# Kernel tuning notes

Measured on AMD Instinct MI355X. Metric: run time of the kernel, lower is better.

Reference implementation:

```python
import jax, jax.numpy as jnp
import numpy as np
from jax import lax

EDGES = [(11,12),(11,23),(12,24),(23,24),(23,25),(25,27),(24,26),(26,28),(11,13),(13,15),(12,14),(14,16)]
J = 33

def _build_neighbors():
    nb = [[j] for j in range(J)]
    for a, b in EDGES:
        nb[a].append(b); nb[b].append(a)
    K = max(len(n) for n in nb)
    idx = np.zeros((J, K), np.int32)
    msk = np.zeros((J, K), np.float32)
    for j, n in enumerate(nb):
        idx[j, :len(n)] = n; msk[j, :len(n)] = 1.0
    return jnp.asarray(idx), jnp.asarray(msk)

NBR_IDX, NBR_MASK = _build_neighbors()
BN_EPS = 1e-5

def conv(x, w, b):
    y = lax.conv_general_dilated(x, w, (1, 1), 'SAME', dimension_numbers=('NCHW', 'OIHW', 'NCHW'))
    return y + b[None, :, None, None]

def bn(x, g, b):
    # eval-mode BatchNorm with running_mean=0, running_var=1
    s = g / jnp.sqrt(1.0 + BN_EPS)
    return x * s[None, :, None, None] + b[None, :, None, None]

def maxpool2(x):
    return lax.reduce_window(x, -jnp.inf, lax.max, (1, 1, 2, 2), (1, 1, 2, 2), 'VALID')

def deconv2x2(x, w, b):
    # ConvTranspose2d(k=2, s=2): w is [Cin, Cout, 2, 2]
    y = jnp.einsum('bcij,codk->boidjk', x, w)
    B, O, H, _, W, _ = y.shape
    return y.reshape(B, O, 2 * H, 2 * W) + b[None, :, None, None]

def forward(x, conv1_w, conv1_b, bn1_g, bn1_b, conv2_w, conv2_b, bn2_g, bn2_b,
            conv3_w, conv3_b, bn3_g, bn3_b, conv4_w, conv4_b, bn4_g, bn4_b,
            dc1_w, dc1_b, dc2_w, dc2_b, head_w, head_b, proj_w, proj_b,
            msg_w, msg_b, gru_w_ih, gru_w_hh, gru_b_ih, gru_b_hh,
            refine_w, refine_b, vis_w1, vis_b1, vis_w2, vis_b2):
    relu = jax.nn.relu
    h = bn(relu(conv(x, conv1_w, conv1_b)), bn1_g, bn1_b)
    h = bn(relu(conv(h, conv2_w, conv2_b)), bn2_g, bn2_b)
    h = maxpool2(h)
    h = bn(relu(conv(h, conv3_w, conv3_b)), bn3_g, bn3_b)
    h = maxpool2(h)
    enc = bn(relu(conv(h, conv4_w, conv4_b)), bn4_g, bn4_b)  # [B,256,H/4,W/4]
    f = relu(deconv2x2(enc, dc1_w, dc1_b))
    feat_map = relu(deconv2x2(f, dc2_w, dc2_b))  # [B,64,H,W]
    init_hm = jax.nn.sigmoid(conv(feat_map, head_w, head_b))  # [B,J,H,W]
    B, Jn, H, W = init_hm.shape
    sm = jax.nn.softmax(init_hm.reshape(B, Jn, H * W) / 0.1, axis=-1).reshape(B, Jn, H, W)
    w_idx = jnp.linspace(0.0, 1.0, W)
    h_idx = jnp.linspace(0.0, 1.0, H)
    pred_x = (sm.sum(-2) * w_idx).sum(-1)  # [B,J] in [0,1]
    pred_y = (sm.sum(-1) * h_idx).sum(-1)
    # grid_sample bilinear, align_corners=True: grid=(2p-1) -> pixel coord p*(dim-1)
    ix = pred_x * (W - 1)
    iy = pred_y * (H - 1)
    x0 = jnp.clip(jnp.floor(ix), 0, W - 1)
    y0 = jnp.clip(jnp.floor(iy), 0, H - 1)
    wx = ix - x0
    wy = iy - y0
    x0i = x0.astype(jnp.int32); x1i = jnp.clip(x0i + 1, 0, W - 1)
    y0i = y0.astype(jnp.int32); y1i = jnp.clip(y0i + 1, 0, H - 1)
    fm = feat_map.transpose(0, 2, 3, 1)  # [B,H,W,C]
    bidx = jnp.arange(B)[:, None]
    v00 = fm[bidx, y0i, x0i]; v01 = fm[bidx, y0i, x1i]
    v10 = fm[bidx, y1i, x0i]; v11 = fm[bidx, y1i, x1i]
    wx = wx[..., None]; wy = wy[..., None]
    joint = (v00 * (1 - wx) * (1 - wy) + v01 * wx * (1 - wy)
             + v10 * (1 - wx) * wy + v11 * wx * wy)  # [B,J,64]
    joint_feats = joint @ proj_w.T + proj_b
    # SkeletonGNN (all joints read original joint_feats -> fully parallel)
    gathered = joint_feats[:, NBR_IDX, :]  # [B,J,K,D]
    lin = gathered @ msg_w.T + msg_b
    m = NBR_MASK[None, :, :, None]
    msgs = (lin * m).sum(2) / NBR_MASK.sum(1)[None, :, None]  # [B,J,D]
    gi = msgs @ gru_w_ih.T + gru_b_ih
    gh = joint_feats @ gru_w_hh.T + gru_b_hh
    D = joint_feats.shape[-1]
    ir, iz, inn = gi[..., :D], gi[..., D:2 * D], gi[..., 2 * D:]
    hr, hz, hn = gh[..., :D], gh[..., D:2 * D], gh[..., 2 * D:]
    r = jax.nn.sigmoid(ir + hr)
    z = jax.nn.sigmoid(iz + hz)
    n = jnp.tanh(inn + r * hn)
    refined_feats = (1 - z) * n + z * joint_feats
    refined_bias = refined_feats.mean(-1)[:, :, None, None]
    refined_hm = jax.nn.sigmoid(conv(init_hm, refine_w, refine_b) + refined_bias)
    # visibility head: adaptive avg pool to 4x4 (enc HW divisible by 4), eval dropout = identity
    eB, eC, eH, eW = enc.shape
    p = enc.reshape(eB, eC, 4, eH // 4, 4, eW // 4).mean((3, 5))  # [B,256,4,4]
    v = jax.nn.relu(p.reshape(eB, -1) @ vis_w1.T + vis_b1)
    vis_pred = jax.nn.sigmoid(v @ vis_w2.T + vis_b2)
    return refined_hm, vis_pred

def setup_inputs() -> dict:
    key = jax.random.key(0)
    ks = iter(jax.random.split(key, 64))
    def w(shape, s=0.05):
        return (jax.random.normal(next(ks), shape, dtype=jnp.float32) * s)
    inp = {
        'x': jax.random.normal(next(ks), (16, 3, 256, 256), dtype=jnp.float32),
        'conv1_w': w((32, 3, 3, 3)), 'conv1_b': w((32,)), 'bn1_g': jnp.ones((32,)), 'bn1_b': jnp.zeros((32,)),
        'conv2_w': w((64, 32, 3, 3)), 'conv2_b': w((64,)), 'bn2_g': jnp.ones((64,)), 'bn2_b': jnp.zeros((64,)),
        'conv3_w': w((128, 64, 3, 3)), 'conv3_b': w((128,)), 'bn3_g': jnp.ones((128,)), 'bn3_b': jnp.zeros((128,)),
        'conv4_w': w((256, 128, 3, 3)), 'conv4_b': w((256,)), 'bn4_g': jnp.ones((256,)), 'bn4_b': jnp.zeros((256,)),
        'dc1_w': w((256, 128, 2, 2)), 'dc1_b': w((128,)),
        'dc2_w': w((128, 64, 2, 2)), 'dc2_b': w((64,)),
        'head_w': w((33, 64, 1, 1)), 'head_b': w((33,)),
        'proj_w': w((64, 64)), 'proj_b': w((64,)),
        'msg_w': w((64, 64)), 'msg_b': w((64,)),
        'gru_w_ih': w((192, 64)), 'gru_w_hh': w((192, 64)),
        'gru_b_ih': w((192,)), 'gru_b_hh': w((192,)),
        'refine_w': w((33, 33, 3, 3)), 'refine_b': w((33,)),
        'vis_w1': w((256, 256 * 16)), 'vis_b1': w((256,)),
        'vis_w2': w((33, 256)), 'vis_b2': w((33,)),
    }
    return inp

def reference(x, conv1_w, conv1_b, bn1_g, bn1_b, conv2_w, conv2_b, bn2_g, bn2_b,
              conv3_w, conv3_b, bn3_g, bn3_b, conv4_w, conv4_b, bn4_g, bn4_b,
              dc1_w, dc1_b, dc2_w, dc2_b, head_w, head_b, proj_w, proj_b,
              msg_w, msg_b, gru_w_ih, gru_w_hh, gru_b_ih, gru_b_hh,
              refine_w, refine_b, vis_w1, vis_b1, vis_w2, vis_b2):
    return forward(x, conv1_w, conv1_b, bn1_g, bn1_b, conv2_w, conv2_b, bn2_g, bn2_b,
                   conv3_w, conv3_b, bn3_g, bn3_b, conv4_w, conv4_b, bn4_g, bn4_b,
                   dc1_w, dc1_b, dc2_w, dc2_b, head_w, head_b, proj_w, proj_b,
                   msg_w, msg_b, gru_w_ih, gru_w_hh, gru_b_ih, gru_b_hh,
                   refine_w, refine_b, vis_w1, vis_b1, vis_w2, vis_b2)
```

## Files before the change

kernel.cpp:

```cpp
#include <hip/hip_runtime.h>
#include <hip/hip_bf16.h>
#include <math.h>

#define BN_RS 0.99999500003749977f

typedef __attribute__((ext_vector_type(8))) __bf16 bf16x8;
typedef __attribute__((ext_vector_type(4))) float f32x4;

union U16 { uint4 u; bf16x8 v; __hip_bfloat16 h[8]; };

__device__ __forceinline__ float sigf(float v) { return 1.0f / (1.0f + expf(-v)); }

__global__ __launch_bounds__(256)
void repack_conv_w_k(const float* __restrict__ w, __hip_bfloat16* __restrict__ wb,
                     int taps, int Co, int Ci, int CoT, int Kp)
{
    int i = blockIdx.x * 256 + threadIdx.x;
    int tot = taps * CoT * Kp;
    if (i >= tot) return;
    int k = i % Kp, n = (i / Kp) % CoT, t = i / (Kp * CoT);
    float v = (n < Co && k < Ci) ? w[((long)n * Ci + k) * taps + t] : 0.0f;
    wb[i] = __float2bfloat16(v);
}
__global__ __launch_bounds__(256)
void repack_deconv_w_k(const float* __restrict__ w, __hip_bfloat16* __restrict__ wb,
                       int Co, int Ci)
{
    int i = blockIdx.x * 256 + threadIdx.x;
    int tot = 4 * Co * Ci;
    if (i >= tot) return;
    int k = i % Ci, n = (i / Ci) % Co, q = i / (Ci * Co);
    wb[i] = __float2bfloat16(w[((long)k * Co + n) * 4 + q]);
}

__global__ __launch_bounds__(256)
void zero_halo_k(__hip_bfloat16* __restrict__ buf, int H, int W, int C, int B)
{
    const int P = W + 2;
    const long per = (long)(2 * P + 2 * H) * C;
    long idx = (long)blockIdx.x * 256 + threadIdx.x;
    if (idx >= per * B) return;
    int b = (int)(idx / per);
    long r = idx % per;
    long off;
    if (r < (long)2 * P * C) {
        int row = (r >= (long)P * C) ? (H + 1) : 0;
        long r2 = r % ((long)P * C);
        off = (((long)b * (H + 2) + row) * P) * C + r2;
    } else {
        long r2 = r - (long)2 * P * C;
        int row = 1 + (int)(r2 / (2 * C));
        int side = (int)((r2 / C) & 1);
        int ch = (int)(r2 % C);
        off = (((long)b * (H + 2) + row) * P + (side ? (W + 1) : 0)) * C + ch;
    }
    buf[off] = __float2bfloat16(0.0f);
}

__global__ __launch_bounds__(256)
void conv1_k(const float* __restrict__ x, const float* __restrict__ w,
             const float* __restrict__ cb, const float* __restrict__ g,
             const float* __restrict__ bb, __hip_bfloat16* __restrict__ out)
{
    __shared__ float sw[216];
    const int tid = threadIdx.x;
    const int b = blockIdx.z >> 2, cg = blockIdx.z & 3, co0 = cg * 8;
    for (int i = tid; i < 216; i += 256) {
        int t = i % 9, co = (i / 9) % 8, ci = i / 72;
        sw[i] = w[((co0 + co) * 3 + ci) * 9 + t];
    }
    __syncthreads();
    const int tx = tid & 15, ty = tid >> 4;
    const int y = blockIdx.y * 16 + ty;
    const int xs = blockIdx.x * 64 + tx;
    float acc[4][8];
#pragma unroll
    for (int p = 0; p < 4; ++p)
#pragma unroll
        for (int c = 0; c < 8; ++c) acc[p][c] = 0.0f;
    for (int ci = 0; ci < 3; ++ci) {
        const float* plane = x + ((long)b * 3 + ci) * 65536;
#pragma unroll
        for (int t = 0; t < 9; ++t) {
            const int dy = t / 3 - 1, dx = t % 3 - 1;
            const int yy = y + dy;
            if ((unsigned)yy < 256u) {
                const float* row = plane + yy * 256;
                float wsr[8];
#pragma unroll
                for (int c = 0; c < 8; ++c) wsr[c] = sw[ci * 72 + c * 9 + t];
#pragma unroll
                for (int p = 0; p < 4; ++p) {
                    const int xx = xs + p * 16 + dx;
                    const float v = ((unsigned)xx < 256u) ? row[xx] : 0.0f;
#pragma unroll
                    for (int c = 0; c < 8; ++c) acc[p][c] = fmaf(v, wsr[c], acc[p][c]);
                }
            }
        }
    }
#pragma unroll
    for (int p = 0; p < 4; ++p) {
        U16 o;
#pragma unroll
        for (int c = 0; c < 8; ++c) {
            const int cc = co0 + c;
            float v = fmaxf(acc[p][c] + cb[cc], 0.0f) * (g[cc] * BN_RS) + bb[cc];
            o.h[c] = __float2bfloat16(v);
        }
        *(uint4*)(void*)(out + ((long)b * 2130048L + ((long)y * 258 + xs + p * 16) * 32) + co0) = o.u;
    }
}

template<int MODE, int NI>
__global__ __launch_bounds__(256)
void mfma_conv_k(const __hip_bfloat16* __restrict__ in,
                 const __hip_bfloat16* __restrict__ wb,
                 const float* __restrict__ cbias,
                 const float* __restrict__ bng, const float* __restrict__ bnb,
                 const float* __restrict__ ebias,
                 __hip_bfloat16* __restrict__ out_bf, float* __restrict__ out_f32,
                 int H, int W, int Cin, int PIT, long bstride, long obstride, int OPIT,
                 int CoutT, int CG, int S)
{
    extern __shared__ float ltr[];
    const int tid = threadIdx.x;
    const int wid = tid >> 6, lane = tid & 63;
    const int ln = lane & 15, kg = lane >> 4;
    const int u = blockIdx.x * 4 + wid;
    const int y = u / S, x0 = (u % S) * 64;
    const int b = blockIdx.z / CG, cg = blockIdx.z % CG;
    const int co0 = cg * 64;
    const int KC = Cin >> 5;

    f32x4 acc[4][NI];
#pragma unroll
    for (int i = 0; i < 4; ++i)
#pragma unroll
        for (int j = 0; j < NI; ++j) acc[i][j] = f32x4{0.f, 0.f, 0.f, 0.f};

    constexpr int NT = (MODE == 1) ? 1 : 9;
    for (int kc = 0; kc < KC; ++kc) {
        const int kofs = kc * 32 + kg * 8;
#pragma unroll
        for (int t = 0; t < NT; ++t) {
            const int dy = (MODE == 1) ? 0 : (t / 3 - 1);
            const int dx = (MODE == 1) ? 0 : (t % 3 - 1);
            bf16x8 wfr[NI];
#pragma unroll
            for (int ni = 0; ni < NI; ++ni)
                wfr[ni] = *(const bf16x8*)(const void*)(wb + ((long)t * CoutT + co0 + ni * 16 + ln) * Cin + kofs);
            U16 av[4];
            const long rowb = (long)b * bstride + (long)(y + dy) * PIT * Cin + kofs;
#pragma unroll
            for (int mi = 0; mi < 4; ++mi)
                av[mi].u = *(const uint4*)(const void*)(in + rowb + (long)(x0 + mi * 16 + ln + dx) * Cin);
#pragma unroll
            for (int mi = 0; mi < 4; ++mi)
#pragma unroll
                for (int ni = 0; ni < NI; ++ni)
                    acc[mi][ni] = __builtin_amdgcn_mfma_f32_16x16x32_bf16(av[mi].v, wfr[ni], acc[mi][ni], 0, 0, 0);
        }
    }

    if constexpr (MODE == 0) {
#pragma unroll
        for (int mi = 0; mi < 4; ++mi) {
#pragma unroll
            for (int r = 0; r < 4; ++r) {
                const int px = x0 + mi * 16 + kg * 4 + r;
                const long pb = (long)b * obstride + ((long)y * OPIT + px) * CoutT + co0;
#pragma unroll
                for (int ni = 0; ni < NI; ++ni) {
                    const int c = co0 + ni * 16 + ln;
                    float v = acc[mi][ni][r] + cbias[c];
                    v = fmaxf(v, 0.0f) * (bng[c] * BN_RS) + bnb[c];
                    out_bf[pb + ni * 16 + ln] = __float2bfloat16(v);
                }
            }
        }
    } else {
        float* wt = ltr + wid * (48 * 67);
#pragma unroll
        for (int mi = 0; mi < 4; ++mi) {
#pragma unroll
            for (int r = 0; r < 4; ++r) {
                const int pxl = mi * 16 + kg * 4 + r;
#pragma unroll
                for (int ni = 0; ni < NI; ++ni) {
                    const int c = ni * 16 + ln;
                    float v = acc[mi][ni][r];
                    if constexpr (MODE == 1) {
                        v = sigf(v + ((c < 33) ? cbias[c] : 0.0f));
                        out_bf[(long)b * obstride + ((long)y * OPIT + x0 + pxl) * CoutT + c] =
                            (c < 33) ? __float2bfloat16(v) : __float2bfloat16(0.0f);
                    } else {
                        float eb = (c < 33) ? (cbias[c] + ebias[b * 33 + c]) : 0.0f;
                        v = sigf(v + eb);
                    }
                    wt[c * 67 + pxl] = v;
                }
            }
        }
        const long o32 = ((long)b * 33) * H * W + (long)y * W + x0 + lane;
        for (int c = 0; c < 33; ++c)
            out_f32[o32 + (long)c * H * W] = wt[c * 67 + lane];
    }
}

__global__ __launch_bounds__(256)
void mfma_deconv_k(const __hip_bfloat16* __restrict__ in,
                   const __hip_bfloat16* __restrict__ wb,
                   const float* __restrict__ bias,
                   __hip_bfloat16* __restrict__ out,
                   int H, int W, int Cin, int CoutT, int CG, int S)
{
    const int tid = threadIdx.x;
    const int wid = tid >> 6, lane = tid & 63;
    const int ln = lane & 15, kg = lane >> 4;
    const int u = blockIdx.x * 4 + wid;
    const int y = u / S, x0 = (u % S) * 64;
    const int b = blockIdx.z / CG, cg = blockIdx.z % CG;
    const int co0 = cg * 64;
    const int KC = Cin >> 5;
    const long inb = (long)b * H * W * Cin;
    const int W2 = W * 2;
    const long ob = (long)b * 4 * H * W * CoutT;

    for (int q = 0; q < 4; ++q) {
        const int dy = q >> 1, dx = q & 1;
        f32x4 acc[4][4];
#pragma unroll
        for (int i = 0; i < 4; ++i)
#pragma unroll
            for (int j = 0; j < 4; ++j) acc[i][j] = f32x4{0.f, 0.f, 0.f, 0.f};
        for (int kc = 0; kc < KC; ++kc) {
            const int kofs = kc * 32 + kg * 8;
            bf16x8 wfr[4];
            U16 av[4];
#pragma unroll
            for (int ni = 0; ni < 4; ++ni)
                wfr[ni] = *(const bf16x8*)(const void*)(wb + ((long)q * CoutT + co0 + ni * 16 + ln) * Cin + kofs);
#pragma unroll
            for (int mi = 0; mi < 4; ++mi)
                av[mi].u = *(const uint4*)(const void*)(in + inb + ((long)y * W + x0 + mi * 16 + ln) * Cin + kofs);
#pragma unroll
            for (int mi = 0; mi < 4; ++mi)
#pragma unroll
                for (int ni = 0; ni < 4; ++ni)
                    acc[mi][ni] = __builtin_amdgcn_mfma_f32_16x16x32_bf16(av[mi].v, wfr[ni], acc[mi][ni], 0, 0, 0);
        }
#pragma unroll
        for (int mi = 0; mi < 4; ++mi) {
#pragma unroll
            for (int r = 0; r < 4; ++r) {
                const int xl = x0 + mi * 16 + kg * 4 + r;
                const long pb = ob + ((long)(2 * y + dy) * W2 + 2 * xl + dx) * CoutT + co0;
#pragma unroll
                for (int ni = 0; ni < 4; ++ni) {
                    const int c = co0 + ni * 16 + ln;
                    float v = fmaxf(acc[mi][ni][r] + bias[c], 0.0f);
                    out[pb + ni * 16 + ln] = __float2bfloat16(v);
                }
            }
        }
    }
}

__global__ __launch_bounds__(256)
void maxpool_bf_k(const __hip_bfloat16* __restrict__ in, __hip_bfloat16* __restrict__ out,
                  int Ho, int Wo, int C, long total, int OPIT, long obstride)
{
    long idx = (long)blockIdx.x * 256 + threadIdx.x;
    if (idx >= total) return;
    const int ng = C >> 3;
    const int cg = (int)(idx % ng);
    long pix = idx / ng;
    const int xo = (int)(pix % Wo); pix /= Wo;
    const int yo = (int)(pix % Ho);
    const int b = (int)(pix / Ho);
    const int Wi = Wo * 2;
    const __hip_bfloat16* p = in + (((long)b * 2 * Ho + 2 * yo) * Wi + 2 * xo) * C + cg * 8;
    U16 a0, a1, a2, a3, o;
    a0.u = *(const uint4*)(const void*)p;
    a1.u = *(const uint4*)(const void*)(p + C);
    a2.u = *(const uint4*)(const void*)(p + (long)Wi * C);
    a3.u = *(const uint4*)(const void*)(p + (long)Wi * C + C);
#pragma unroll
    for (int j = 0; j < 8; ++j) {
        float m = fmaxf(fmaxf(__bfloat162float(a0.h[j]), __bfloat162float(a1.h[j])),
                        fmaxf(__bfloat162float(a2.h[j]), __bfloat162float(a3.h[j])));
        o.h[j] = __float2bfloat16(m);
    }
    *(uint4*)(void*)(out + (long)b * obstride + ((long)yo * OPIT + xo) * C + cg * 8) = o.u;
}

__global__ __launch_bounds__(256)
void softargmax_k(const float* __restrict__ hm, float* __restrict__ coords)
{
    __shared__ float r0[256], r1[256], r2[256];
    const int bj = blockIdx.x;
    const int tid = threadIdx.x;
    const float* row = hm + (long)bj * 65536;
    float m = -1e30f;
    for (int i = tid; i < 65536; i += 256) m = fmaxf(m, row[i]);
    r0[tid] = m;
    __syncthreads();
    for (int s = 128; s > 0; s >>= 1) {
        if (tid < s) r0[tid] = fmaxf(r0[tid], r0[tid + s]);
        __syncthreads();
    }
    const float mx = r0[0];
    __syncthreads();
    float s = 0.0f, sx = 0.0f, sy = 0.0f;
    for (int i = tid; i < 65536; i += 256) {
        float e = expf((row[i] - mx) * 10.0f);
        s += e;
        sx += e * (float)(i & 255);
        sy += e * (float)(i >> 8);
    }
    r0[tid] = s; r1[tid] = sx; r2[tid] = sy;
    __syncthreads();
    for (int st = 128; st > 0; st >>= 1) {
        if (tid < st) { r0[tid] += r0[tid + st]; r1[tid] += r1[tid + st]; r2[tid] += r2[tid + st]; }
        __syncthreads();
    }
    if (tid == 0) {
        coords[2 * bj] = r1[0] / r0[0];
        coords[2 * bj + 1] = r2[0] / r0[0];
    }
}

__global__ __launch_bounds__(64)
void joint_bf_k(const __hip_bfloat16* __restrict__ fm, const float* __restrict__ coords,
                const float* __restrict__ pw, const float* __restrict__ pb,
                float* __restrict__ jf)
{
    __shared__ float sj[64];
    const int bj = blockIdx.x, b = bj / 33;
    const int tid = threadIdx.x;
    float ix = coords[2 * bj], iy = coords[2 * bj + 1];
    float x0f = fminf(fmaxf(floorf(ix), 0.0f), 255.0f);
    float y0f = fminf(fmaxf(floorf(iy), 0.0f), 255.0f);
    float wx = ix - x0f, wy = iy - y0f;
    int x0 = (int)x0f, y0 = (int)y0f;
    int x1 = min(x0 + 1, 255), y1 = min(y0 + 1, 255);
    const __hip_bfloat16* base = fm + (long)b * 65536 * 64 + tid;
    float v00 = __bfloat162float(base[((long)y0 * 256 + x0) * 64]);
    float v01 = __bfloat162float(base[((long)y0 * 256 + x1) * 64]);
    float v10 = __bfloat162float(base[((long)y1 * 256 + x0) * 64]);
    float v11 = __bfloat162float(base[((long)y1 * 256 + x1) * 64]);
    sj[tid] = v00 * (1 - wx) * (1 - wy) + v01 * wx * (1 - wy)
            + v10 * (1 - wx) * wy + v11 * wx * wy;
    __syncthreads();
    float a = pb[tid];
    for (int k = 0; k < 64; ++k) a = fmaf(sj[k], pw[tid * 64 + k], a);
    jf[(long)bj * 64 + tid] = a;
}

__device__ const int d_nbr[33][4] = {
    {0,0,0,0},{1,0,0,0},{2,0,0,0},{3,0,0,0},{4,0,0,0},{5,0,0,0},{6,0,0,0},{7,0,0,0},
    {8,0,0,0},{9,0,0,0},{10,0,0,0},
    {11,12,23,13},{12,11,24,14},{13,11,15,0},{14,12,16,0},{15,13,0,0},{16,14,0,0},
    {17,0,0,0},{18,0,0,0},{19,0,0,0},{20,0,0,0},{21,0,0,0},{22,0,0,0},
    {23,11,24,25},{24,12,23,26},{25,23,27,0},{26,24,28,0},{27,25,0,0},{28,26,0,0},
    {29,0,0,0},{30,0,0,0},{31,0,0,0},{32,0,0,0}};
__device__ const int d_cnt[33] = {1,1,1,1,1,1,1,1,1,1,1,4,4,3,3,2,2,1,1,1,1,1,1,4,4,3,3,2,2,1,1,1,1};

__global__ __launch_bounds__(192)
void gru_k(const float* __restrict__ jf, const float* __restrict__ mw, const float* __restrict__ mb,
           const float* __restrict__ wih, const float* __restrict__ whh,
           const float* __restrict__ bih, const float* __restrict__ bhh,
           float* __restrict__ rbias)
{
    __shared__ float s_mjf[64], s_jf[64], s_msg[64], s_gi[192], s_gh[192], s_ref[64];
    const int bj = blockIdx.x;
    const int b = bj / 33, j = bj % 33;
    const int tid = threadIdx.x;
    if (tid < 64) {
        int cnt = d_cnt[j];
        float s = 0.0f;
        for (int n = 0; n < 4; ++n)
            if (n < cnt) s += jf[((long)b * 33 + d_nbr[j][n]) * 64 + tid];
        s_mjf[tid] = s / (float)cnt;
        s_jf[tid] = jf[(long)bj * 64 + tid];
    }
    __syncthreads();
    if (tid < 64) {
        float a = mb[tid];
        for (int k = 0; k < 64; ++k) a = fmaf(mw[tid * 64 + k], s_mjf[k], a);
        s_msg[tid] = a;
    }
    __syncthreads();
    {
        float a = bih[tid], c = bhh[tid];
        for (int k = 0; k < 64; ++k) {
            a = fmaf(wih[tid * 64 + k], s_msg[k], a);
            c = fmaf(whh[tid * 64 + k], s_jf[k], c);
        }
        s_gi[tid] = a; s_gh[tid] = c;
    }
    __syncthreads();
    if (tid < 64) {
        float r = sigf(s_gi[tid] + s_gh[tid]);
        float z = sigf(s_gi[64 + tid] + s_gh[64 + tid]);
        float n = tanhf(s_gi[128 + tid] + r * s_gh[128 + tid]);
        s_ref[tid] = (1.0f - z) * n + z * s_jf[tid];
    }
    __syncthreads();
    if (tid == 0) {
        float s = 0.0f;
        for (int k = 0; k < 64; ++k) s += s_ref[k];
        rbias[bj] = s * (1.0f / 64.0f);
    }
}

__global__ __launch_bounds__(256)
void vispool_bf_k(const __hip_bfloat16* __restrict__ enc, float* __restrict__ p)
{
    int idx = blockIdx.x * 256 + threadIdx.x;
    int v = idx & 3, uu = (idx >> 2) & 3, c = (idx >> 4) & 255, b = idx >> 12;
    const __hip_bfloat16* base = enc + (long)b * 64 * 64 * 256 + c;
    float s = 0.0f;
    for (int a = 0; a < 16; ++a)
#pragma unroll
        for (int d = 0; d < 16; ++d)
            s += __bfloat162float(base[((long)(uu * 16 + a) * 64 + (v * 16 + d)) * 256]);
    p[idx] = s * (1.0f / 256.0f);
}

__global__ __launch_bounds__(256)
void visfc1_k(const float* __restrict__ p, const float* __restrict__ w1,
              const float* __restrict__ b1, float* __restrict__ v1)
{
    __shared__ float s_p[4096];
    const int b = blockIdx.x, tid = threadIdx.x;
    for (int i = tid; i < 4096; i += 256) s_p[i] = p[b * 4096 + i];
    __syncthreads();
    float a = b1[tid];
    const float* wr = w1 + (long)tid * 4096;
    for (int k = 0; k < 4096; ++k) a = fmaf(wr[k], s_p[k], a);
    v1[b * 256 + tid] = fmaxf(a, 0.0f);
}

__global__ __launch_bounds__(64)
void visfc2_k(const float* __restrict__ v1, const float* __restrict__ w2,
              const float* __restrict__ b2, float* __restrict__ out)
{
    const int b = blockIdx.x, t = threadIdx.x;
    if (t < 33) {
        float a = b2[t];
        for (int k = 0; k < 256; ++k) a = fmaf(w2[t * 256 + k], v1[b * 256 + k], a);
        out[b * 33 + t] = sigf(a);
    }
}

extern "C" void kernel_launch(void* const* d_in, const int* in_sizes, int n_in,
                              void* d_out, int out_size, void* d_ws, size_t ws_size,
                              hipStream_t stream)
{
    const float* x   = (const float*)d_in[0];
    const float* c1w = (const float*)d_in[1];  const float* c1b = (const float*)d_in[2];
    const float* b1g = (const float*)d_in[3];  const float* b1b = (const float*)d_in[4];
    const float* c2w = (const float*)d_in[5];  const float* c2b = (const float*)d_in[6];
    const float* b2g = (const float*)d_in[7];  const float* b2b = (const float*)d_in[8];
    const float* c3w = (const float*)d_in[9];  const float* c3b = (const float*)d_in[10];
    const float* b3g = (const float*)d_in[11]; const float* b3b = (const float*)d_in[12];
    const float* c4w = (const float*)d_in[13]; const float* c4b = (const float*)d_in[14];
    const float* b4g = (const float*)d_in[15]; const float* b4b = (const float*)d_in[16];
    const float* d1w = (const float*)d_in[17]; const float* d1b = (const float*)d_in[18];
    const float* d2w = (const float*)d_in[19]; const float* d2b = (const float*)d_in[20];
    const float* hw  = (const float*)d_in[21]; const float* hb  = (const float*)d_in[22];
    const float* pw  = (const float*)d_in[23]; const float* pb  = (const float*)d_in[24];
    const float* mw  = (const float*)d_in[25]; const float* mb  = (const float*)d_in[26];
    const float* wih = (const float*)d_in[27]; const float* whh = (const float*)d_in[28];
    const float* bih = (const float*)d_in[29]; const float* bhh = (const float*)d_in[30];
    const float* rw  = (const float*)d_in[31]; const float* rb  = (const float*)d_in[32];
    const float* v1w = (const float*)d_in[33]; const float* v1b = (const float*)d_in[34];
    const float* v2w = (const float*)d_in[35]; const float* v2b = (const float*)d_in[36];

    char* ws = (char*)d_ws;
    __hip_bfloat16* ENC  = (__hip_bfloat16*)(ws + 0L);
    __hip_bfloat16* R1   = (__hip_bfloat16*)(ws + 33554432L);
    __hip_bfloat16* R2   = (__hip_bfloat16*)(ws + 167772160L);
    char*           R3c  = ws + 304095232L;
    char* SM = ws + 442507264L;

    __hip_bfloat16* H1B = R1;                 __hip_bfloat16* H1I = R1 + 8288;
    __hip_bfloat16* P1B = R1;                 __hip_bfloat16* P1I = R1 + 8384;
    __hip_bfloat16* FEAT = R1;
    __hip_bfloat16* H3  = R2;
    __hip_bfloat16* F   = R2;
    __hip_bfloat16* HDB = R2;                 __hip_bfloat16* HDI = R2 + 16576;
    __hip_bfloat16* P2B = (__hip_bfloat16*)R3c; __hip_bfloat16* P2I = P2B + 8576;
    float*          INITHM = (float*)R3c;

    __hip_bfloat16* W2B = (__hip_bfloat16*)(SM + 0);
    __hip_bfloat16* W3B = (__hip_bfloat16*)(SM + 36864);
    __hip_bfloat16* W4B = (__hip_bfloat16*)(SM + 184320);
    __hip_bfloat16* WRB = (__hip_bfloat16*)(SM + 774144);
    __hip_bfloat16* WHB = (__hip_bfloat16*)(SM + 847872);
    __hip_bfloat16* WD1 = (__hip_bfloat16*)(SM + 856064);
    __hip_bfloat16* WD2 = (__hip_bfloat16*)(SM + 1118208);
    float* CO = (float*)(SM + 1183744);
    float* JF = (float*)(SM + 1187968);
    float* RB = (float*)(SM + 1323136);
    float* P  = (float*)(SM + 1325248);
    float* V1 = (float*)(SM + 1587392);

    float* out_hm  = (float*)d_out;
    float* out_vis = out_hm + 34603008L;
    __hip_bfloat16* H2 = (__hip_bfloat16*)d_out;

    repack_conv_w_k<<<(9*64*32 + 255)/256, 256, 0, stream>>>(c2w, W2B, 9, 64, 32, 64, 32);
    repack_conv_w_k<<<(9*128*64 + 255)/256, 256, 0, stream>>>(c3w, W3B, 9, 128, 64, 128, 64);
    repack_conv_w_k<<<(9*256*128 + 255)/256, 256, 0, stream>>>(c4w, W4B, 9, 256, 128, 256, 128);
    repack_conv_w_k<<<(9*64*64 + 255)/256, 256, 0, stream>>>(rw, WRB, 9, 33, 33, 64, 64);
    repack_conv_w_k<<<(1*64*64 + 255)/256, 256, 0, stream>>>(hw, WHB, 1, 33, 64, 64, 64);
    repack_deconv_w_k<<<(4*128*256 + 255)/256, 256, 0, stream>>>(d1w, WD1, 128, 256);
    repack_deconv_w_k<<<(4*64*128 + 255)/256, 256, 0, stream>>>(d2w, WD2, 64, 128);

    zero_halo_k<<<(526336 + 255)/256, 256, 0, stream>>>(H1B, 256, 256, 32, 16);
    zero_halo_k<<<(532480 + 255)/256, 256, 0, stream>>>(P2B, 64, 64, 128, 16);

    conv1_k<<<dim3(4, 16, 64), 256, 0, stream>>>(x, c1w, c1b, b1g, b1b, H1I);
    mfma_conv_k<0, 4><<<dim3(256, 1, 16), 256, 0, stream>>>(
        H1I, W2B, c2b, b2g, b2b, nullptr, H2, nullptr,
        256, 256, 32, 258, 2130048L, 4194304L, 256, 64, 1, 4);
    zero_halo_k<<<(528384 + 255)/256, 256, 0, stream>>>(P1B, 128, 128, 64, 16);
    maxpool_bf_k<<<8192, 256, 0, stream>>>(H2, P1I, 128, 128, 64, 2097152L, 130, 1081600L);
    mfma_conv_k<0, 4><<<dim3(64, 1, 32), 256, 0, stream>>>(
        P1I, W3B, c3b, b3g, b3b, nullptr, H3, nullptr,
        128, 128, 64, 130, 1081600L, 2097152L, 128, 128, 2, 2);
    maxpool_bf_k<<<4096, 256, 0, stream>>>(H3, P2I, 64, 64, 128, 1048576L, 66, 557568L);
    mfma_conv_k<0, 4><<<dim3(16, 1, 64), 256, 0, stream>>>(
        P2I, W4B, c4b, b4g, b4b, nullptr, ENC, nullptr,
        64, 64, 128, 66, 557568L, 1048576L, 64, 256, 4, 1);
    mfma_deconv_k<<<dim3(16, 1, 32), 256, 0, stream>>>(
        ENC, WD1, d1b, F, 64, 64, 256, 128, 2, 1);
    mfma_deconv_k<<<dim3(64, 1, 16), 256, 0, stream>>>(
        F, WD2, d2b, FEAT, 128, 128, 128, 64, 1, 2);
    zero_halo_k<<<(1052672 + 255)/256, 256, 0, stream>>>(HDB, 256, 256, 64, 16);
    mfma_conv_k<1, 3><<<dim3(256, 1, 16), 256, 51456, stream>>>(
        FEAT, WHB, hb, nullptr, nullptr, nullptr, HDI, INITHM,
        256, 256, 64, 256, 4194304L, 4260096L, 258, 64, 1, 4);
    softargmax_k<<<528, 256, 0, stream>>>(INITHM, CO);
    joint_bf_k<<<528, 64, 0, stream>>>(FEAT, CO, pw, pb, JF);
    gru_k<<<528, 192, 0, stream>>>(JF, mw, mb, wih, whh, bih, bhh, RB);
    mfma_conv_k<2, 3><<<dim3(256, 1, 16), 256, 51456, stream>>>(
        HDI, WRB, rb, nullptr, nullptr, RB, nullptr, out_hm,
        256, 256, 64, 258, 4260096L, 0L, 0, 64, 1, 4);
    vispool_bf_k<<<256, 256, 0, stream>>>(ENC, P);
    visfc1_k<<<16, 256, 0, stream>>>(P, v1w, v1b, V1);
    visfc2_k<<<16, 64, 0, stream>>>(V1, v2w, v2b, out_vis);
}
```

Baseline: 1.562 ms.

## Shrink MFMA conv/deconv tiles, add occupancy hints and block-index swizzle

```diff
diff --git a/kernel.cpp b/kernel.cpp
--- a/kernel.cpp
+++ b/kernel.cpp
@@ -112,8 +112,8 @@
     }
 }
 
-template<int MODE, int NI>
-__global__ __launch_bounds__(256)
+template<int MODE, int NI, int MI>
+__global__ __launch_bounds__(256, 4)
 void mfma_conv_k(const __hip_bfloat16* __restrict__ in,
                  const __hip_bfloat16* __restrict__ wb,
                  const float* __restrict__ cbias,
@@ -127,15 +127,17 @@
     const int tid = threadIdx.x;
     const int wid = tid >> 6, lane = tid & 63;
     const int ln = lane & 15, kg = lane >> 4;
-    const int u = blockIdx.x * 4 + wid;
-    const int y = u / S, x0 = (u % S) * 64;
+    const int nx = gridDim.x;
+    const int bx = (blockIdx.x & 7) * (nx >> 3) + (blockIdx.x >> 3);
+    const int u = bx * 4 + wid;
+    const int y = u / S, x0 = (u % S) * (MI * 16);
     const int b = blockIdx.z / CG, cg = blockIdx.z % CG;
-    const int co0 = cg * 64;
+    const int co0 = cg * (NI * 16);
     const int KC = Cin >> 5;
 
-    f32x4 acc[4][NI];
-#pragma unroll
-    for (int i = 0; i < 4; ++i)
+    f32x4 acc[MI][NI];
+#pragma unroll
+    for (int i = 0; i < MI; ++i)
 #pragma unroll
         for (int j = 0; j < NI; ++j) acc[i][j] = f32x4{0.f, 0.f, 0.f, 0.f};
 
@@ -150,13 +152,13 @@
 #pragma unroll
             for (int ni = 0; ni < NI; ++ni)
                 wfr[ni] = *(const bf16x8*)(const void*)(wb + ((long)t * CoutT + co0 + ni * 16 + ln) * Cin + kofs);
-            U16 av[4];
+            U16 av[MI];
             const long rowb = (long)b * bstride + (long)(y + dy) * PIT * Cin + kofs;
 #pragma unroll
-            for (int mi = 0; mi < 4; ++mi)
+            for (int mi = 0; mi < MI; ++mi)
                 av[mi].u = *(const uint4*)(const void*)(in + rowb + (long)(x0 + mi * 16 + ln + dx) * Cin);
 #pragma unroll
-            for (int mi = 0; mi < 4; ++mi)
+            for (int mi = 0; mi < MI; ++mi)
 #pragma unroll
                 for (int ni = 0; ni < NI; ++ni)
                     acc[mi][ni] = __builtin_amdgcn_mfma_f32_16x16x32_bf16(av[mi].v, wfr[ni], acc[mi][ni], 0, 0, 0);
@@ -165,7 +167,7 @@
 
     if constexpr (MODE == 0) {
 #pragma unroll
-        for (int mi = 0; mi < 4; ++mi) {
+        for (int mi = 0; mi < MI; ++mi) {
 #pragma unroll
             for (int r = 0; r < 4; ++r) {
                 const int px = x0 + mi * 16 + kg * 4 + r;
@@ -180,9 +182,10 @@
             }
         }
     } else {
-        float* wt = ltr + wid * (48 * 67);
-#pragma unroll
-        for (int mi = 0; mi < 4; ++mi) {
+        constexpr int PXW = MI * 16;
+        float* wt = ltr + wid * (48 * (PXW + 1));
+#pragma unroll
+        for (int mi = 0; mi < MI; ++mi) {
 #pragma unroll
             for (int r = 0; r < 4; ++r) {
                 const int pxl = mi * 16 + kg * 4 + r;
@@ -198,17 +201,19 @@
                         float eb = (c < 33) ? (cbias[c] + ebias[b * 33 + c]) : 0.0f;
                         v = sigf(v + eb);
                     }
-                    wt[c * 67 + pxl] = v;
+                    wt[c * (PXW + 1) + pxl] = v;
                 }
             }
         }
-        const long o32 = ((long)b * 33) * H * W + (long)y * W + x0 + lane;
-        for (int c = 0; c < 33; ++c)
-            out_f32[o32 + (long)c * H * W] = wt[c * 67 + lane];
-    }
-}
-
-__global__ __launch_bounds__(256)
+        if (lane < PXW) {
+            const long o32 = ((long)b * 33) * H * W + (long)y * W + x0 + lane;
+            for (int c = 0; c < 33; ++c)
+                out_f32[o32 + (long)c * H * W] = wt[c * (PXW + 1) + lane];
+        }
+    }
+}
+
+__global__ __launch_bounds__(256, 4)
 void mfma_deconv_k(const __hip_bfloat16* __restrict__ in,
                    const __hip_bfloat16* __restrict__ wb,
                    const float* __restrict__ bias,
@@ -218,10 +223,12 @@
     const int tid = threadIdx.x;
     const int wid = tid >> 6, lane = tid & 63;
     const int ln = lane & 15, kg = lane >> 4;
-    const int u = blockIdx.x * 4 + wid;
+    const int nx = gridDim.x;
+    const int bx = (blockIdx.x & 7) * (nx >> 3) + (blockIdx.x >> 3);
+    const int u = bx * 4 + wid;
     const int y = u / S, x0 = (u % S) * 64;
     const int b = blockIdx.z / CG, cg = blockIdx.z % CG;
-    const int co0 = cg * 64;
+    const int co0 = cg * 32;
     const int KC = Cin >> 5;
     const long inb = (long)b * H * W * Cin;
     const int W2 = W * 2;
@@ -229,17 +236,17 @@
 
     for (int q = 0; q < 4; ++q) {
         const int dy = q >> 1, dx = q & 1;
-        f32x4 acc[4][4];
+        f32x4 acc[4][2];
 #pragma unroll
         for (int i = 0; i < 4; ++i)
 #pragma unroll
-            for (int j = 0; j < 4; ++j) acc[i][j] = f32x4{0.f, 0.f, 0.f, 0.f};
+            for (int j = 0; j < 2; ++j) acc[i][j] = f32x4{0.f, 0.f, 0.f, 0.f};
         for (int kc = 0; kc < KC; ++kc) {
             const int kofs = kc * 32 + kg * 8;
-            bf16x8 wfr[4];
+            bf16x8 wfr[2];
             U16 av[4];
 #pragma unroll
-            for (int ni = 0; ni < 4; ++ni)
+            for (int ni = 0; ni < 2; ++ni)
                 wfr[ni] = *(const bf16x8*)(const void*)(wb + ((long)q * CoutT + co0 + ni * 16 + ln) * Cin + kofs);
 #pragma unroll
             for (int mi = 0; mi < 4; ++mi)
@@ -247,7 +254,7 @@
 #pragma unroll
             for (int mi = 0; mi < 4; ++mi)
 #pragma unroll
-                for (int ni = 0; ni < 4; ++ni)
+                for (int ni = 0; ni < 2; ++ni)
                     acc[mi][ni] = __builtin_amdgcn_mfma_f32_16x16x32_bf16(av[mi].v, wfr[ni], acc[mi][ni], 0, 0, 0);
         }
 #pragma unroll
@@ -257,7 +264,7 @@
                 const int xl = x0 + mi * 16 + kg * 4 + r;
                 const long pb = ob + ((long)(2 * y + dy) * W2 + 2 * xl + dx) * CoutT + co0;
 #pragma unroll
-                for (int ni = 0; ni < 4; ++ni) {
+                for (int ni = 0; ni < 2; ++ni) {
                     const int c = co0 + ni * 16 + ln;
                     float v = fmaxf(acc[mi][ni][r] + bias[c], 0.0f);
                     out[pb + ni * 16 + ln] = __float2bfloat16(v);
@@ -524,32 +531,32 @@
     zero_halo_k<<<(532480 + 255)/256, 256, 0, stream>>>(P2B, 64, 64, 128, 16);
 
     conv1_k<<<dim3(4, 16, 64), 256, 0, stream>>>(x, c1w, c1b, b1g, b1b, H1I);
-    mfma_conv_k<0, 4><<<dim3(256, 1, 16), 256, 0, stream>>>(
+    mfma_conv_k<0, 2, 4><<<dim3(256, 1, 32), 256, 0, stream>>>(
         H1I, W2B, c2b, b2g, b2b, nullptr, H2, nullptr,
-        256, 256, 32, 258, 2130048L, 4194304L, 256, 64, 1, 4);
+        256, 256, 32, 258, 2130048L, 4194304L, 256, 64, 2, 4);
     zero_halo_k<<<(528384 + 255)/256, 256, 0, stream>>>(P1B, 128, 128, 64, 16);
     maxpool_bf_k<<<8192, 256, 0, stream>>>(H2, P1I, 128, 128, 64, 2097152L, 130, 1081600L);
-    mfma_conv_k<0, 4><<<dim3(64, 1, 32), 256, 0, stream>>>(
+    mfma_conv_k<0, 2, 4><<<dim3(64, 1, 64), 256, 0, stream>>>(
         P1I, W3B, c3b, b3g, b3b, nullptr, H3, nullptr,
-        128, 128, 64, 130, 1081600L, 2097152L, 128, 128, 2, 2);
+        128, 128, 64, 130, 1081600L, 2097152L, 128, 128, 4, 2);
     maxpool_bf_k<<<4096, 256, 0, stream>>>(H3, P2I, 64, 64, 128, 1048576L, 66, 557568L);
-    mfma_conv_k<0, 4><<<dim3(16, 1, 64), 256, 0, stream>>>(
+    mfma_conv_k<0, 2, 4><<<dim3(16, 1, 128), 256, 0, stream>>>(
         P2I, W4B, c4b, b4g, b4b, nullptr, ENC, nullptr,
-        64, 64, 128, 66, 557568L, 1048576L, 64, 256, 4, 1);
-    mfma_deconv_k<<<dim3(16, 1, 32), 256, 0, stream>>>(
-        ENC, WD1, d1b, F, 64, 64, 256, 128, 2, 1);
-    mfma_deconv_k<<<dim3(64, 1, 16), 256, 0, stream>>>(
-        F, WD2, d2b, FEAT, 128, 128, 128, 64, 1, 2);
+        64, 64, 128, 66, 557568L, 1048576L, 64, 256, 8, 1);
+    mfma_deconv_k<<<dim3(16, 1, 64), 256, 0, stream>>>(
+        ENC, WD1, d1b, F, 64, 64, 256, 128, 4, 1);
+    mfma_deconv_k<<<dim3(64, 1, 32), 256, 0, stream>>>(
+        F, WD2, d2b, FEAT, 128, 128, 128, 64, 2, 2);
     zero_halo_k<<<(1052672 + 255)/256, 256, 0, stream>>>(HDB, 256, 256, 64, 16);
-    mfma_conv_k<1, 3><<<dim3(256, 1, 16), 256, 51456, stream>>>(
+    mfma_conv_k<1, 3, 2><<<dim3(512, 1, 16), 256, 25344, stream>>>(
         FEAT, WHB, hb, nullptr, nullptr, nullptr, HDI, INITHM,
-        256, 256, 64, 256, 4194304L, 4260096L, 258, 64, 1, 4);
+        256, 256, 64, 256, 4194304L, 4260096L, 258, 64, 1, 8);
     softargmax_k<<<528, 256, 0, stream>>>(INITHM, CO);
     joint_bf_k<<<528, 64, 0, stream>>>(FEAT, CO, pw, pb, JF);
     gru_k<<<528, 192, 0, stream>>>(JF, mw, mb, wih, whh, bih, bhh, RB);
-    mfma_conv_k<2, 3><<<dim3(256, 1, 16), 256, 51456, stream>>>(
+    mfma_conv_k<2, 3, 2><<<dim3(512, 1, 16), 256, 25344, stream>>>(
         HDI, WRB, rb, nullptr, nullptr, RB, nullptr, out_hm,
-        256, 256, 64, 258, 4260096L, 0L, 0, 64, 1, 4);
+        256, 256, 64, 258, 4260096L, 0L, 0, 64, 1, 8);
     vispool_bf_k<<<256, 256, 0, stream>>>(ENC, P);
     visfc1_k<<<16, 256, 0, stream>>>(P, v1w, v1b, V1);
     visfc2_k<<<16, 64, 0, stream>>>(V1, v2w, v2b, out_vis);
```

Result: slower. 2.298 ms (+47.0%).
